# Performance work log

Measured on AMD Instinct MI355X. Metric: run time of the kernel, lower is better.

The kernel has to match this reference:

```python
import jax, jax.numpy as jnp
import numpy as np

N_POINTS = 2_000_000
GRID = 256  # voxel grid resolution (D=H=W), production-scale stand-in for source's 128


def setup_inputs() -> dict:
    key = jax.random.key(0)
    k1, k2, k3 = jax.random.split(key, 3)
    coords = jax.random.uniform(k1, (N_POINTS, 3), dtype=jnp.float32,
                                minval=-0.95, maxval=0.95)
    registration_pred = jax.random.normal(k2, (N_POINTS, 3), dtype=jnp.float32) * 0.02
    registration_gt = jax.random.normal(k3, (N_POINTS, 3), dtype=jnp.float32) * 0.02
    return {"registration_pred": registration_pred,
            "registration_gt": registration_gt,
            "coords": coords}


def _splat(pts, size):
    """Trilinear scatter (adjoint of F.grid_sample, align_corners=False,
    zero padding). pts: [N,3] normalized coords in (x,y,z) order mapping to
    (W,H,D). Splats weight 1 per point. Returns [D,H,W] volume."""
    D = H = W = size
    # grid_sample align_corners=False unnormalization: p = ((g+1)*size - 1)/2
    x = ((pts[:, 0] + 1.0) * W - 1.0) * 0.5
    y = ((pts[:, 1] + 1.0) * H - 1.0) * 0.5
    z = ((pts[:, 2] + 1.0) * D - 1.0) * 0.5
    x0f, y0f, z0f = jnp.floor(x), jnp.floor(y), jnp.floor(z)
    fx, fy, fz = x - x0f, y - y0f, z - z0f  # fractional offsets
    x0, y0, z0 = x0f.astype(jnp.int32), y0f.astype(jnp.int32), z0f.astype(jnp.int32)
    vol = jnp.zeros(D * H * W, dtype=pts.dtype)
    for dz in (0, 1):
        wz = fz if dz else (1.0 - fz)
        for dy in (0, 1):
            wy = fy if dy else (1.0 - fy)
            for dx in (0, 1):
                wx = fx if dx else (1.0 - fx)
                xi, yi, zi = x0 + dx, y0 + dy, z0 + dz
                valid = ((xi >= 0) & (xi < W) & (yi >= 0) & (yi < H)
                         & (zi >= 0) & (zi < D))
                w = jnp.where(valid, wx * wy * wz, 0.0)
                idx = jnp.where(valid, (zi * H + yi) * W + xi, 0)
                vol = vol.at[idx].add(w)
    return vol.reshape(D, H, W)


def reference(registration_pred, registration_gt, coords):
    pred_vol = _splat(coords + registration_pred, GRID)
    gt_vol = _splat(coords + registration_gt, GRID)
    # HuberLoss(reduction='sum', delta=1.0)
    d = pred_vol - gt_vol
    ad = jnp.abs(d)
    return jnp.sum(jnp.where(ad <= 1.0, 0.5 * d * d, ad - 0.5))
```

## Files before the change

kernel.cpp:

```cpp
#include <hip/hip_runtime.h>

#define GRID_RES 256
#define NCELLS 1024
#define NB 1024
#define BCAP 6144
#define NPT 2

#define W_SCALE 2097152.0f
#define INV_W (1.0f / 2097152.0f)
#define L_SCALE 512.0f
#define INV_L (1.0f / 512.0f)

struct CEv { unsigned w0, w1q, xyz; };

__device__ __forceinline__ CEv make_cev(float px, float py, float pz,
                                        unsigned sign) {
    float x = ((px + 1.0f) * (float)GRID_RES - 1.0f) * 0.5f;
    float y = ((py + 1.0f) * (float)GRID_RES - 1.0f) * 0.5f;
    float z = ((pz + 1.0f) * (float)GRID_RES - 1.0f) * 0.5f;
    float xf = floorf(x), yf = floorf(y), zf = floorf(z);
    int x0 = (int)xf, y0 = (int)yf, z0 = (int)zf;
    unsigned qx = (unsigned)((x - xf) * 65535.0f + 0.5f);
    unsigned qy = (unsigned)((y - yf) * 65535.0f + 0.5f);
    unsigned qz = (unsigned)((z - zf) * 16383.0f + 0.5f);
    bool valid = (x0 >= -1) & (x0 <= 255) & (y0 >= -1) & (y0 <= 255) &
                 (z0 >= -1) & (z0 <= 255);
    CEv e;
    e.w0 = qx | (qy << 16);
    e.w1q = qz | (sign << 31);
    e.xyz = valid ? ((unsigned)(x0 + 1) | ((unsigned)(y0 + 1) << 10) |
                     ((unsigned)(z0 + 1) << 20) | (1u << 30))
                  : 0u;
    return e;
}

template <typename F>
__device__ __forceinline__ void enum_cells(const CEv& e, F&& emit) {
    if (!(e.xyz & (1u << 30))) return;
    int x0 = (int)(e.xyz & 1023u) - 1;
    int y0 = (int)((e.xyz >> 10) & 1023u) - 1;
    int z0 = (int)((e.xyz >> 20) & 1023u) - 1;
    int cxs[2], cys[2], czs[2];
    int nx = 0, ny = 0, nz = 0;
    {
        bool vA = (x0 >= 0) & (x0 <= 255);
        bool vB = (x0 >= -1) & (x0 <= 254);
        int cA = x0 >> 5, cB = (x0 + 1) >> 5;
        if (vA) cxs[nx++] = cA;
        if (vB && (!vA || cB != cA)) cxs[nx++] = cB;
    }
    {
        bool vA = (y0 >= 0) & (y0 <= 255);
        bool vB = (y0 >= -1) & (y0 <= 254);
        int cA = y0 >> 5, cB = (y0 + 1) >> 5;
        if (vA) cys[ny++] = cA;
        if (vB && (!vA || cB != cA)) cys[ny++] = cB;
    }
    {
        bool vA = (z0 >= 0) & (z0 <= 255);
        bool vB = (z0 >= -1) & (z0 <= 254);
        int cA = z0 >> 4, cB = (z0 + 1) >> 4;
        if (vA) czs[nz++] = cA;
        if (vB && (!vA || cB != cA)) czs[nz++] = cB;
    }
    for (int a = 0; a < nz; ++a) {
        int cz = czs[a];
        unsigned lz = (unsigned)(z0 - (cz << 4) + 1);
        for (int b = 0; b < ny; ++b) {
            int cy = cys[b];
            unsigned ly = (unsigned)(y0 - (cy << 5) + 1);
            for (int c = 0; c < nx; ++c) {
                int cx = cxs[c];
                unsigned lx = (unsigned)(x0 - (cx << 5) + 1);
                int cell = (cz << 6) | (cy << 3) | cx;
                unsigned w1 = e.w1q | (lx << 14) | (ly << 20) | (lz << 26);
                emit(cell, e.w0, w1);
            }
        }
    }
}

__global__ __launch_bounds__(1024) void bin_kernel(
    const float* __restrict__ pred, const float* __restrict__ gt,
    const float* __restrict__ coords, unsigned* __restrict__ segOff,
    unsigned* __restrict__ segCnt, uint2* __restrict__ payload,
    int* __restrict__ lossAcc, int n) {
    __shared__ unsigned h[NCELLS];
    __shared__ unsigned wtot[16];
    int b = blockIdx.x;
    int t = threadIdx.x;
    if (b == 0 && t == 0) lossAcc[0] = 0;
    h[t] = 0;
    __syncthreads();

    int chunk = (n + NB - 1) / NB;
    int start = b * chunk;
    int end = min(start + chunk, n);
    const float3* c3 = (const float3*)coords;
    const float3* p3 = (const float3*)pred;
    const float3* g3 = (const float3*)gt;

    CEv ev[2 * NPT];
#pragma unroll
    for (int k = 0; k < NPT; ++k) {
        int i = start + t + (k << 10);
        if (i < end) {
            float3 c = c3[i];
            float3 p = p3[i];
            float3 g = g3[i];
            ev[2 * k] = make_cev(c.x + p.x, c.y + p.y, c.z + p.z, 0u);
            ev[2 * k + 1] = make_cev(c.x + g.x, c.y + g.y, c.z + g.z, 1u);
        } else {
            ev[2 * k].xyz = 0;
            ev[2 * k + 1].xyz = 0;
        }
    }

#pragma unroll
    for (int k = 0; k < 2 * NPT; ++k)
        enum_cells(ev[k], [&](int cell, unsigned, unsigned) {
            atomicAdd(&h[cell], 1u);
        });
    __syncthreads();

    unsigned x = h[t];
    unsigned incl = x;
    int lane = t & 63, wid = t >> 6;
#pragma unroll
    for (int off = 1; off < 64; off <<= 1) {
        unsigned y = __shfl_up(incl, off, 64);
        if (lane >= off) incl += y;
    }
    if (lane == 63) wtot[wid] = incl;
    __syncthreads();
    if (t == 0) {
        unsigned r = 0;
#pragma unroll
        for (int w = 0; w < 16; ++w) { unsigned v = wtot[w]; wtot[w] = r; r += v; }
    }
    __syncthreads();
    unsigned offE = incl - x + wtot[wid];
    segOff[(size_t)b * NCELLS + t] = offE;
    segCnt[(size_t)b * NCELLS + t] = x;
    __syncthreads();
    h[t] = offE;
    __syncthreads();

    uint2* pb = payload + (size_t)b * BCAP;
#pragma unroll
    for (int k = 0; k < 2 * NPT; ++k)
        enum_cells(ev[k], [&](int cell, unsigned w0, unsigned w1) {
            unsigned slot = atomicAdd(&h[cell], 1u);
            if (slot < (unsigned)BCAP) pb[slot] = make_uint2(w0, w1);
        });
}

__global__ __launch_bounds__(1024) void accum_kernel(
    const uint2* __restrict__ payload, const unsigned* __restrict__ segOff,
    const unsigned* __restrict__ segCnt, int* __restrict__ lossAcc) {
    __shared__ int v[16384];
    __shared__ unsigned sbase[NB + 1];
    __shared__ unsigned pbase[NB];
    __shared__ unsigned w16[16];
    __shared__ float wsum[16];
    int c = blockIdx.x;
    int t = threadIdx.x;
#pragma unroll
    for (int j = 0; j < 16; ++j) v[t + (j << 10)] = 0;

    int lane = t & 63, wid = t >> 6;
    unsigned cnt = segCnt[(size_t)t * NCELLS + c];
    unsigned off = segOff[(size_t)t * NCELLS + c];
    unsigned incl = cnt;
#pragma unroll
    for (int o = 1; o < 64; o <<= 1) {
        unsigned y = __shfl_up(incl, o, 64);
        if (lane >= o) incl += y;
    }
    if (lane == 63) w16[wid] = incl;
    __syncthreads();
    if (t == 0) {
        unsigned r = 0;
#pragma unroll
        for (int w = 0; w < 16; ++w) { unsigned q = w16[w]; w16[w] = r; r += q; }
        sbase[NB] = r;
    }
    __syncthreads();
    if (t == 0) sbase[NB] = w16[15] + incl - cnt + cnt;
    __syncthreads();
    sbase[t] = incl - cnt + w16[wid];
    pbase[t] = (unsigned)t * (unsigned)BCAP + off;
    if (t == 1023) sbase[NB] = incl + w16[wid];
    __syncthreads();

    unsigned total = sbase[NB];
    for (unsigned i = t; i < total; i += 1024) {
        int lo = 0, hi = NB - 1;
#pragma unroll
        for (int s = 0; s < 10; ++s) {
            int mid = (lo + hi + 1) >> 1;
            if (sbase[mid] <= i) lo = mid; else hi = mid - 1;
        }
        uint2 p = payload[(size_t)pbase[lo] + (i - sbase[lo])];
        float fx = (float)(p.x & 0xFFFFu) * (1.0f / 65535.0f);
        float fy = (float)(p.x >> 16) * (1.0f / 65535.0f);
        float fz = (float)(p.y & 0x3FFFu) * (1.0f / 16383.0f);
        int lx = (int)((p.y >> 14) & 63u);
        int ly = (int)((p.y >> 20) & 63u);
        int lz = (int)((p.y >> 26) & 31u);
        float s = (p.y >> 31) ? -W_SCALE : W_SCALE;
        float wxs[2] = {1.0f - fx, fx};
        float wys[2] = {1.0f - fy, fy};
        float wzs[2] = {1.0f - fz, fz};
        int xb = lx - 1, yb = ly - 1, zb = lz - 1;
#pragma unroll
        for (int dz = 0; dz < 2; ++dz) {
            int rz = zb + dz;
            if ((unsigned)rz > 15u) continue;
            float wz = s * wzs[dz];
#pragma unroll
            for (int dy = 0; dy < 2; ++dy) {
                int ry = yb + dy;
                if ((unsigned)ry > 31u) continue;
                float wyz = wz * wys[dy];
#pragma unroll
                for (int dx = 0; dx < 2; ++dx) {
                    int rx = xb + dx;
                    if ((unsigned)rx > 31u) continue;
                    int iw = __float2int_rn(wyz * wxs[dx]);
                    atomicAdd(&v[(rz << 10) | (ry << 5) | rx], iw);
                }
            }
        }
    }
    __syncthreads();

    float acc = 0.0f;
#pragma unroll
    for (int j = 0; j < 16; ++j) {
        int val = v[t + (j << 10)];
        float d = (float)val * INV_W;
        float ad = fabsf(d);
        acc += (ad <= 1.0f) ? 0.5f * d * d : ad - 0.5f;
    }
#pragma unroll
    for (int o = 32; o > 0; o >>= 1) acc += __shfl_down(acc, o, 64);
    if (lane == 0) wsum[wid] = acc;
    __syncthreads();
    if (t == 0) {
        float tsum = 0.0f;
#pragma unroll
        for (int w = 0; w < 16; ++w) tsum += wsum[w];
        atomicAdd(lossAcc, __float2int_rn(tsum * L_SCALE));
    }
}

__global__ void finalize_kernel(const int* __restrict__ lossAcc,
                                float* __restrict__ out) {
    out[0] = (float)lossAcc[0] * INV_L;
}

extern "C" void kernel_launch(void* const* d_in, const int* in_sizes, int n_in,
                              void* d_out, int out_size, void* d_ws, size_t ws_size,
                              hipStream_t stream) {
    const float* reg_pred = (const float*)d_in[0];
    const float* reg_gt   = (const float*)d_in[1];
    const float* coords   = (const float*)d_in[2];
    float* out = (float*)d_out;

    char* ws = (char*)d_ws;
    int* lossAcc = (int*)ws;
    unsigned* segOff = (unsigned*)(ws + 256);
    unsigned* segCnt = segOff + (size_t)NB * NCELLS;
    uint2* payload = (uint2*)((char*)segCnt + (size_t)NB * NCELLS * 4);

    int n = in_sizes[0] / 3;

    bin_kernel<<<NB, 1024, 0, stream>>>(reg_pred, reg_gt, coords, segOff,
                                        segCnt, payload, lossAcc, n);
    accum_kernel<<<NCELLS, 1024, 0, stream>>>(payload, segOff, segCnt,
                                              lossAcc);
    finalize_kernel<<<1, 1, 0, stream>>>(lossAcc, out);
}
```

Before: 166.8 us.

## Stage bin payload in LDS, pack segment table, replace binary search with item map

The bin kernel now scatters payload entries into a shared-memory buffer and copies them out to global memory with coalesced 16-byte stores, instead of doing scattered global writes. Segment offset and count are packed into one 32-bit word, which halves the table traffic in both kernels. The accum kernel builds a per-item segment index in LDS, replacing the per-item 10-step binary search, and clears and reads the voxel array with int4 accesses. The costs are more LDS use, which may lower occupancy, and a new ISEGCAP cap on items per cell that silently drops entries above it.

```diff
diff --git a/kernel.cpp b/kernel.cpp
--- a/kernel.cpp
+++ b/kernel.cpp
@@ -5,6 +5,7 @@
 #define NB 1024
 #define BCAP 6144
 #define NPT 2
+#define ISEGCAP 5888
 
 #define W_SCALE 2097152.0f
 #define INV_W (1.0f / 2097152.0f)
@@ -82,11 +83,13 @@
 
 __global__ __launch_bounds__(1024) void bin_kernel(
     const float* __restrict__ pred, const float* __restrict__ gt,
-    const float* __restrict__ coords, unsigned* __restrict__ segOff,
-    unsigned* __restrict__ segCnt, uint2* __restrict__ payload,
-    int* __restrict__ lossAcc, int n) {
+    const float* __restrict__ coords, unsigned* __restrict__ segTab,
+    uint2* __restrict__ payload, int* __restrict__ lossAcc, int n) {
     __shared__ unsigned h[NCELLS];
     __shared__ unsigned wtot[16];
+    __shared__ unsigned totalS;
+    __shared__ uint4 plq[BCAP / 2];
+    uint2* pl = (uint2*)plq;
     int b = blockIdx.x;
     int t = threadIdx.x;
     if (b == 0 && t == 0) lossAcc[0] = 0;
@@ -137,40 +140,48 @@
         unsigned r = 0;
 #pragma unroll
         for (int w = 0; w < 16; ++w) { unsigned v = wtot[w]; wtot[w] = r; r += v; }
+        totalS = r;
     }
     __syncthreads();
     unsigned offE = incl - x + wtot[wid];
-    segOff[(size_t)b * NCELLS + t] = offE;
-    segCnt[(size_t)b * NCELLS + t] = x;
-    __syncthreads();
+    segTab[(size_t)b * NCELLS + t] = (offE << 16) | x;
     h[t] = offE;
     __syncthreads();
 
-    uint2* pb = payload + (size_t)b * BCAP;
 #pragma unroll
     for (int k = 0; k < 2 * NPT; ++k)
         enum_cells(ev[k], [&](int cell, unsigned w0, unsigned w1) {
             unsigned slot = atomicAdd(&h[cell], 1u);
-            if (slot < (unsigned)BCAP) pb[slot] = make_uint2(w0, w1);
+            if (slot < (unsigned)BCAP) pl[slot] = make_uint2(w0, w1);
         });
+    __syncthreads();
+
+    unsigned tot = totalS;
+    unsigned m = min((tot + 1u) >> 1, (unsigned)(BCAP / 2));
+    uint4* gp4 = (uint4*)(payload + (size_t)b * BCAP);
+    for (unsigned i = t; i < m; i += 1024) gp4[i] = plq[i];
 }
 
 __global__ __launch_bounds__(1024) void accum_kernel(
-    const uint2* __restrict__ payload, const unsigned* __restrict__ segOff,
-    const unsigned* __restrict__ segCnt, int* __restrict__ lossAcc) {
-    __shared__ int v[16384];
-    __shared__ unsigned sbase[NB + 1];
-    __shared__ unsigned pbase[NB];
+    const uint2* __restrict__ payload, const unsigned* __restrict__ segTab,
+    int* __restrict__ lossAcc) {
+    __shared__ int4 v4s[4096];
+    __shared__ unsigned short itemSeg[ISEGCAP];
+    __shared__ unsigned pbs[NB];
     __shared__ unsigned w16[16];
     __shared__ float wsum[16];
+    __shared__ unsigned totalS;
+    int* v = (int*)v4s;
     int c = blockIdx.x;
     int t = threadIdx.x;
-#pragma unroll
-    for (int j = 0; j < 16; ++j) v[t + (j << 10)] = 0;
-
+    int4 z; z.x = 0; z.y = 0; z.z = 0; z.w = 0;
+#pragma unroll
+    for (int j = 0; j < 4; ++j) v4s[t + (j << 10)] = z;
+
+    unsigned tab = segTab[(size_t)t * NCELLS + c];
+    unsigned cnt = tab & 0xFFFFu;
+    unsigned off = tab >> 16;
     int lane = t & 63, wid = t >> 6;
-    unsigned cnt = segCnt[(size_t)t * NCELLS + c];
-    unsigned off = segOff[(size_t)t * NCELLS + c];
     unsigned incl = cnt;
 #pragma unroll
     for (int o = 1; o < 64; o <<= 1) {
@@ -183,25 +194,21 @@
         unsigned r = 0;
 #pragma unroll
         for (int w = 0; w < 16; ++w) { unsigned q = w16[w]; w16[w] = r; r += q; }
-        sbase[NB] = r;
-    }
-    __syncthreads();
-    if (t == 0) sbase[NB] = w16[15] + incl - cnt + cnt;
-    __syncthreads();
-    sbase[t] = incl - cnt + w16[wid];
-    pbase[t] = (unsigned)t * (unsigned)BCAP + off;
-    if (t == 1023) sbase[NB] = incl + w16[wid];
-    __syncthreads();
-
-    unsigned total = sbase[NB];
+        totalS = r;
+    }
+    __syncthreads();
+    unsigned base = incl - cnt + w16[wid];
+    pbs[t] = (unsigned)t * (unsigned)BCAP + off - base;
+    for (unsigned k = 0; k < cnt; ++k) {
+        unsigned idx = base + k;
+        if (idx < (unsigned)ISEGCAP) itemSeg[idx] = (unsigned short)t;
+    }
+    __syncthreads();
+
+    unsigned total = min(totalS, (unsigned)ISEGCAP);
     for (unsigned i = t; i < total; i += 1024) {
-        int lo = 0, hi = NB - 1;
-#pragma unroll
-        for (int s = 0; s < 10; ++s) {
-            int mid = (lo + hi + 1) >> 1;
-            if (sbase[mid] <= i) lo = mid; else hi = mid - 1;
-        }
-        uint2 p = payload[(size_t)pbase[lo] + (i - sbase[lo])];
+        unsigned seg = itemSeg[i];
+        uint2 p = payload[(size_t)(unsigned)(pbs[seg] + i)];
         float fx = (float)(p.x & 0xFFFFu) * (1.0f / 65535.0f);
         float fy = (float)(p.x >> 16) * (1.0f / 65535.0f);
         float fz = (float)(p.y & 0x3FFFu) * (1.0f / 16383.0f);
@@ -237,11 +244,28 @@
 
     float acc = 0.0f;
 #pragma unroll
-    for (int j = 0; j < 16; ++j) {
-        int val = v[t + (j << 10)];
-        float d = (float)val * INV_W;
-        float ad = fabsf(d);
-        acc += (ad <= 1.0f) ? 0.5f * d * d : ad - 0.5f;
+    for (int j = 0; j < 4; ++j) {
+        int4 q = v4s[t + (j << 10)];
+        {
+            float d = (float)q.x * INV_W;
+            float ad = fabsf(d);
+            acc += (ad <= 1.0f) ? 0.5f * d * d : ad - 0.5f;
+        }
+        {
+            float d = (float)q.y * INV_W;
+            float ad = fabsf(d);
+            acc += (ad <= 1.0f) ? 0.5f * d * d : ad - 0.5f;
+        }
+        {
+            float d = (float)q.z * INV_W;
+            float ad = fabsf(d);
+            acc += (ad <= 1.0f) ? 0.5f * d * d : ad - 0.5f;
+        }
+        {
+            float d = (float)q.w * INV_W;
+            float ad = fabsf(d);
+            acc += (ad <= 1.0f) ? 0.5f * d * d : ad - 0.5f;
+        }
     }
 #pragma unroll
     for (int o = 32; o > 0; o >>= 1) acc += __shfl_down(acc, o, 64);
@@ -270,15 +294,13 @@
 
     char* ws = (char*)d_ws;
     int* lossAcc = (int*)ws;
-    unsigned* segOff = (unsigned*)(ws + 256);
-    unsigned* segCnt = segOff + (size_t)NB * NCELLS;
-    uint2* payload = (uint2*)((char*)segCnt + (size_t)NB * NCELLS * 4);
+    unsigned* segTab = (unsigned*)(ws + 256);
+    uint2* payload = (uint2*)(ws + 256 + (size_t)NB * NCELLS * 4);
 
     int n = in_sizes[0] / 3;
 
-    bin_kernel<<<NB, 1024, 0, stream>>>(reg_pred, reg_gt, coords, segOff,
-                                        segCnt, payload, lossAcc, n);
-    accum_kernel<<<NCELLS, 1024, 0, stream>>>(payload, segOff, segCnt,
-                                              lossAcc);
+    bin_kernel<<<NB, 1024, 0, stream>>>(reg_pred, reg_gt, coords, segTab,
+                                        payload, lossAcc, n);
+    accum_kernel<<<NCELLS, 1024, 0, stream>>>(payload, segTab, lossAcc);
     finalize_kernel<<<1, 1, 0, stream>>>(lossAcc, out);
 }
```

Result: faster. 156.3 us (-6.3%).
